# Performance work log

Measured on AMD Instinct MI355X. Metric: run time of the kernel, lower is better.

Reference implementation:

```python
import jax, jax.numpy as jnp
import numpy as np

B, S, D, H, DQ, DK = 2, 2048, 1024, 16, 64, 64


def setup_inputs() -> dict:
    key = jax.random.key(0)
    ks = jax.random.split(key, 11)
    s = 0.02
    return {
        "query": jax.random.normal(ks[0], (B, S, D), jnp.float32),
        "key": jax.random.normal(ks[1], (B, S, D), jnp.float32),
        "value": jax.random.normal(ks[2], (B, S, D), jnp.float32),
        "Wq": jax.random.normal(ks[3], (H, D, DQ), jnp.float32) * s,
        "bq": jax.random.normal(ks[4], (H, DQ), jnp.float32) * s,
        "Wk": jax.random.normal(ks[5], (H, D, DK), jnp.float32) * s,
        "bk": jax.random.normal(ks[6], (H, DK), jnp.float32) * s,
        "Wv": jax.random.normal(ks[7], (H, D, DK), jnp.float32) * s,
        "bv": jax.random.normal(ks[8], (H, DK), jnp.float32) * s,
        "Wo": jax.random.normal(ks[9], (H * DK, D), jnp.float32) * s,
        "bo": jax.random.normal(ks[10], (D,), jnp.float32) * s,
    }


def reference(query, key, value, Wq, bq, Wk, bk, Wv, bv, Wo, bo):
    # Per-head linear projections (batched over heads): [B,H,S,dq/dk]
    q = jnp.einsum('bsd,hde->bhse', query, Wq) + bq[None, :, None, :]
    k = jnp.einsum('bsd,hde->bhse', key, Wk) + bk[None, :, None, :]
    v = jnp.einsum('bsd,hde->bhse', value, Wv) + bv[None, :, None, :]
    # Scaled dot-product attention: softmax(QK^T / sqrt(dim_q)) V
    scale = 1.0 / jnp.sqrt(jnp.asarray(q.shape[-1], q.dtype))
    scores = jnp.einsum('bhse,bhte->bhst', q, k) * scale  # [B,H,S,S]
    attn = jax.nn.softmax(scores, axis=-1)
    out = jnp.einsum('bhst,bhte->bhse', attn, v)  # [B,H,S,dk]
    # Concat heads along feature dim, then output linear
    cat = out.transpose(0, 2, 1, 3).reshape(out.shape[0], out.shape[2], -1)  # [B,S,H*dk]
    return cat @ Wo + bo
```

## Files before the change

### kernel.cpp

```cpp
#include <hip/hip_runtime.h>
#include <hip/hip_bf16.h>
#include <math.h>

#define NB 2
#define NS 2048
#define ND 1024
#define NH 16
#define DH 64
#define MROWS (NB*NS)
#define NCOLS (NH*DH)

typedef __attribute__((ext_vector_type(8))) short bf16x8;
typedef __attribute__((ext_vector_type(4))) float f32x4;
typedef __attribute__((ext_vector_type(4))) unsigned short ushort4t;
typedef __attribute__((ext_vector_type(8))) unsigned short ushort8t;
typedef unsigned short ushort;

extern "C" __device__ float __ocml_native_exp2_f32(float);
#define EXP2F(x) __ocml_native_exp2_f32(x)
#define LOG2E 1.44269504088896f

static __device__ __forceinline__ ushort f2bf(float f) {
    union { __hip_bfloat16 b; ushort u; } cv;
    cv.b = __hip_bfloat16(f);
    return cv.u;
}

static __device__ __forceinline__ void gld_lds16(const void* g, void* l) {
    __builtin_amdgcn_global_load_lds(
        (const __attribute__((address_space(1))) void*)g,
        (__attribute__((address_space(3))) void*)l, 16, 0, 0);
}

__global__ __launch_bounds__(256) void convert_x(
    const float* __restrict__ q, const float* __restrict__ k,
    const float* __restrict__ v, ushort* __restrict__ X_bf)
{
    const size_t n1 = (size_t)MROWS * ND;
    const size_t off = ((size_t)blockIdx.x * 256 + threadIdx.x) * 8;
    const float* srcs[3] = {q, k, v};
    #pragma unroll
    for (int p = 0; p < 3; ++p) {
        float4 a = *(const float4*)(srcs[p] + off);
        float4 b = *(const float4*)(srcs[p] + off + 4);
        ushort8t w;
        w[0]=f2bf(a.x); w[1]=f2bf(a.y); w[2]=f2bf(a.z); w[3]=f2bf(a.w);
        w[4]=f2bf(b.x); w[5]=f2bf(b.y); w[6]=f2bf(b.z); w[7]=f2bf(b.w);
        *(ushort8t*)(X_bf + (size_t)p * n1 + off) = w;
    }
}

__global__ __launch_bounds__(256) void repack_w(
    const float* __restrict__ Wq, const float* __restrict__ Wk,
    const float* __restrict__ Wv, ushort* __restrict__ WT_bf)
{
    const int p = blockIdx.z;
    const float* W = (p == 0) ? Wq : (p == 1) ? Wk : Wv;
    const int h = blockIdx.y, d0 = blockIdx.x * 64;
    __shared__ float tile[64][65];
    const int t = threadIdx.x;
    {
        const int i = t >> 2, e0 = (t & 3) * 16;
        const float* src = W + ((size_t)h * ND + d0 + i) * DH + e0;
        #pragma unroll
        for (int u = 0; u < 4; ++u) {
            float4 v4 = ((const float4*)src)[u];
            tile[i][e0 + u*4 + 0] = v4.x; tile[i][e0 + u*4 + 1] = v4.y;
            tile[i][e0 + u*4 + 2] = v4.z; tile[i][e0 + u*4 + 3] = v4.w;
        }
    }
    __syncthreads();
    {
        const int e = t >> 2, dc = (t & 3) * 16;
        ushort* dst = WT_bf + ((size_t)p * NCOLS + h * 64 + e) * ND + d0 + dc;
        ushort8t w0, w1;
        #pragma unroll
        for (int u = 0; u < 8; ++u) { w0[u] = f2bf(tile[dc+u][e]); w1[u] = f2bf(tile[dc+8+u][e]); }
        *(ushort8t*)dst = w0;
        *(ushort8t*)(dst + 8) = w1;
    }
}

__global__ __launch_bounds__(256) void repack_wo(
    const float* __restrict__ Wo, ushort* __restrict__ WoT_bf)
{
    const int f0 = blockIdx.x * 64, c0 = blockIdx.y * 64;
    __shared__ float tile[64][65];
    const int t = threadIdx.x;
    {
        const int i = t >> 2, j0 = (t & 3) * 16;
        const float* src = Wo + (size_t)(f0 + i) * ND + c0 + j0;
        #pragma unroll
        for (int u = 0; u < 4; ++u) {
            float4 v4 = ((const float4*)src)[u];
            tile[i][j0 + u*4 + 0] = v4.x; tile[i][j0 + u*4 + 1] = v4.y;
            tile[i][j0 + u*4 + 2] = v4.z; tile[i][j0 + u*4 + 3] = v4.w;
        }
    }
    __syncthreads();
    {
        const int cl = t >> 2, fc = (t & 3) * 16;
        ushort* dst = WoT_bf + (size_t)(c0 + cl) * ND + f0 + fc;
        ushort8t w0, w1;
        #pragma unroll
        for (int u = 0; u < 8; ++u) { w0[u] = f2bf(tile[fc+u][cl]); w1[u] = f2bf(tile[fc+8+u][cl]); }
        *(ushort8t*)dst = w0;
        *(ushort8t*)(dst + 8) = w1;
    }
}

__global__ __launch_bounds__(256) void gemm_qkv(
    const ushort* __restrict__ X_bf, const ushort* __restrict__ WT_bf,
    const float* __restrict__ bq, const float* __restrict__ bk,
    const float* __restrict__ bv, ushort* __restrict__ qkv_bf)
{
    const int p = blockIdx.z;
    const float* bias = (p == 0) ? bq : (p == 1) ? bk : bv;
    const float scale = (p == 0) ? 0.125f * LOG2E : 1.0f;
    const int m0 = blockIdx.x * 128, n0 = blockIdx.y * 128;
    const int t = threadIdx.x, wid = t >> 6, lane = t & 63;
    const int wr = wid >> 1, wc = wid & 1;
    const int c = lane & 15, g = lane >> 4;

    __shared__ ushort ldsA[128 * 64];
    __shared__ ushort ldsB[128 * 64];

    const ushort* Ag = X_bf + (size_t)p * MROWS * ND + (size_t)m0 * ND;
    const ushort* Bg = WT_bf + (size_t)p * NCOLS * ND + (size_t)n0 * ND;

    f32x4 acc[4][4];
    #pragma unroll
    for (int m = 0; m < 4; ++m)
        #pragma unroll
        for (int n = 0; n < 4; ++n)
            acc[m][n] = (f32x4){0.f, 0.f, 0.f, 0.f};

    for (int k0 = 0; k0 < ND; k0 += 64) {
        __syncthreads();
        #pragma unroll
        for (int call = 0; call < 4; ++call) {
            const int chb = wid * 256 + call * 64;
            const int ch = chb + lane;
            const int row = ch >> 3, c16 = ch & 7;
            gld_lds16(Ag + (size_t)row * ND + k0 + c16 * 8, ldsA + (size_t)ch * 8);
            gld_lds16(Bg + (size_t)row * ND + k0 + c16 * 8, ldsB + (size_t)ch * 8);
        }
        __syncthreads();
        #pragma unroll
        for (int kc = 0; kc < 2; ++kc) {
            bf16x8 af[4], bfr[4];
            #pragma unroll
            for (int m = 0; m < 4; ++m)
                af[m] = *(const bf16x8*)(ldsA + (wr*64 + m*16 + c) * 64 + kc*32 + g*8);
            #pragma unroll
            for (int n = 0; n < 4; ++n)
                bfr[n] = *(const bf16x8*)(ldsB + (wc*64 + n*16 + c) * 64 + kc*32 + g*8);
            #pragma unroll
            for (int m = 0; m < 4; ++m)
                #pragma unroll
                for (int n = 0; n < 4; ++n)
                    acc[m][n] = __builtin_amdgcn_mfma_f32_16x16x32_bf16(af[m], bfr[n], acc[m][n], 0, 0, 0);
        }
    }

    ushort* dst = qkv_bf + (size_t)p * ((size_t)NB * NH * NS * DH);
    #pragma unroll
    for (int m = 0; m < 4; ++m) {
        const int gr0 = m0 + wr*64 + m*16 + g*4;
        #pragma unroll
        for (int n = 0; n < 4; ++n) {
            const int gc = n0 + wc*64 + n*16 + c;
            const int h = gc >> 6, e = gc & 63;
            const float bv_ = bias[gc];
            #pragma unroll
            for (int j = 0; j < 4; ++j) {
                const int r = gr0 + j;
                const int b = r >> 11, s = r & (NS - 1);
                dst[(((size_t)b * NH + h) * NS + s) * DH + e] = f2bf((acc[m][n][j] + bv_) * scale);
            }
        }
    }
}

__global__ __launch_bounds__(256) void v_transpose(
    const ushort* __restrict__ v_bf, ushort* __restrict__ vT_bf)
{
    const int bh = blockIdx.y, s0 = blockIdx.x * 256;
    __shared__ ushort tile[256][72];
    const int t = threadIdx.x;
    const ushort* src = v_bf + ((size_t)bh * NS + s0) * DH;
    #pragma unroll
    for (int u = 0; u < 8; ++u) {
        const int idx = u * 256 + t;
        const int row = idx >> 3, cc = (idx & 7) * 8;
        *(ushort8t*)&tile[row][cc] = *(const ushort8t*)(src + (size_t)row * DH + cc);
    }
    __syncthreads();
    const int e = t >> 2, sc = (t & 3) * 64;
    ushort* dst = vT_bf + ((size_t)bh * DH + e) * NS + s0 + sc;
    #pragma unroll
    for (int u = 0; u < 8; ++u) {
        ushort8t w;
        #pragma unroll
        for (int x = 0; x < 8; ++x) w[x] = tile[sc + u*8 + x][e];
        *(ushort8t*)(dst + u * 8) = w;
    }
}

__global__ __launch_bounds__(256) void attn_kernel(
    const ushort* __restrict__ q_bf, const ushort* __restrict__ k_bf,
    const ushort* __restrict__ vT_bf, ushort* __restrict__ cat_bf)
{
    __shared__ __attribute__((aligned(16))) char smem[40960];
    const int t = threadIdx.x;
    const int wid = t >> 6, lane = t & 63;
    const int g = lane >> 4, c = lane & 15;
    const int bh = blockIdx.y;
    const int qrow0 = blockIdx.x * 64 + wid * 16;

    bf16x8 qf[2];
    {
        const char* qp = (const char*)(q_bf + ((size_t)bh * NS + qrow0 + c) * DH);
        qf[0] = *(const bf16x8*)(qp + g * 16);
        qf[1] = *(const bf16x8*)(qp + 64 + g * 16);
    }

    f32x4 o_acc[4];
    const f32x4 zero = {0.f, 0.f, 0.f, 0.f};
    #pragma unroll
    for (int n = 0; n < 4; ++n) o_acc[n] = zero;
    float m[4], lsum[4];
    #pragma unroll
    for (int r = 0; r < 4; ++r) { m[r] = -INFINITY; lsum[r] = 0.f; }

    const char* kg = (const char*)(k_bf + (size_t)bh * NS * DH);
    const char* vg = (const char*)(vT_bf + (size_t)bh * DH * NS);

    const int ch0 = t * 2;
    const int row0 = ch0 >> 3, c16a = ch0 & 7;
    const int row1 = (ch0 + 1) >> 3, c16b = (ch0 + 1) & 7;
    const int swz0 = (c16a * 16) ^ ((row0 & 7) << 4);
    const int swz1 = (c16b * 16) ^ ((row1 & 7) << 4);

    ushort8t kr0, kr1, vr0, vr1;

    #define ATTN_LOAD(JT) do { \
        kr0 = *(const ushort8t*)(kg + (size_t)((JT) + row0) * 128 + c16a * 16); \
        kr1 = *(const ushort8t*)(kg + (size_t)((JT) + row1) * 128 + c16b * 16); \
        vr0 = *(const ushort8t*)(vg + (size_t)row0 * (NS*2) + (size_t)((JT) + c16a*8) * 2); \
        vr1 = *(const ushort8t*)(vg + (size_t)row1 * (NS*2) + (size_t)((JT) + c16b*8) * 2); \
    } while (0)

    #define ATTN_STORE(BUF) do { \
        char* Kd = smem + (BUF) * 8192; \
        char* Vd = smem + 16384 + (BUF) * 8192; \
        *(ushort8t*)(Kd + row0 * 128 + swz0) = kr0; \
        *(ushort8t*)(Kd + row1 * 128 + swz1) = kr1; \
        *(ushort8t*)(Vd + row0 * 128 + swz0) = vr0; \
        *(ushort8t*)(Vd + row1 * 128 + swz1) = vr1; \
    } while (0)

    ATTN_LOAD(0);
    ATTN_STORE(0);
    __syncthreads();
    int cur = 0;
    char* Ps = smem + 32768 + wid * 2048;

    for (int jt = 0; jt < NS; jt += 64) {
        ATTN_LOAD((jt + 64) & (NS - 1));

        const char* Ks  = smem + cur * 8192;
        const char* VTs = smem + 16384 + cur * 8192;

        f32x4 s_acc[4];
        #pragma unroll
        for (int n = 0; n < 4; ++n) s_acc[n] = zero;
        __builtin_amdgcn_s_setprio(1);
        #pragma unroll
        for (int n = 0; n < 4; ++n) {
            const int key = n * 16 + c;
            #pragma unroll
            for (int kc = 0; kc < 2; ++kc) {
                bf16x8 kf = *(const bf16x8*)(Ks + key * 128 + ((kc * 64 + g * 16) ^ ((key & 7) << 4)));
                s_acc[n] = __builtin_amdgcn_mfma_f32_16x16x32_bf16(qf[kc], kf, s_acc[n], 0, 0, 0);
            }
        }
        __builtin_amdgcn_s_setprio(0);

        float pv[4][4];
        #pragma unroll
        for (int r = 0; r < 4; ++r) {
            float tm = fmaxf(fmaxf(s_acc[0][r], s_acc[1][r]), fmaxf(s_acc[2][r], s_acc[3][r]));
            if (!__all(tm <= m[r] + 11.5f)) {
                tm = fmaxf(tm, __shfl_xor(tm, 1));
                tm = fmaxf(tm, __shfl_xor(tm, 2));
                tm = fmaxf(tm, __shfl_xor(tm, 4));
                tm = fmaxf(tm, __shfl_xor(tm, 8));
                const float mnew = fmaxf(m[r], tm);
                const float sc = EXP2F(m[r] - mnew);
                lsum[r] *= sc;
                o_acc[0][r] *= sc; o_acc[1][r] *= sc;
                o_acc[2][r] *= sc; o_acc[3][r] *= sc;
                m[r] = mnew;
            }
            float rs = 0.f;
            #pragma unroll
            for (int n = 0; n < 4; ++n) {
                float pj = EXP2F(s_acc[n][r] - m[r]);
                pv[n][r] = pj;
                rs += pj;
            }
            lsum[r] += rs;
        }

        #pragma unroll
        for (int n = 0; n < 4; ++n) {
            #pragma unroll
            for (int r = 0; r < 4; ++r) {
                const int q = g * 4 + r;
                *(ushort*)(Ps + q * 128 + ((n * 32 + c * 2) ^ ((q & 7) << 4))) = f2bf(pv[n][r]);
            }
        }

        __builtin_amdgcn_s_setprio(1);
        #pragma unroll
        for (int kc = 0; kc < 2; ++kc) {
            bf16x8 pa = *(const bf16x8*)(Ps + c * 128 + ((kc * 64 + g * 16) ^ ((c & 7) << 4)));
            #pragma unroll
            for (int n = 0; n < 4; ++n) {
                const int e = n * 16 + c;
                bf16x8 vf = *(const bf16x8*)(VTs + e * 128 + ((kc * 64 + g * 16) ^ ((e & 7) << 4)));
                o_acc[n] = __builtin_amdgcn_mfma_f32_16x16x32_bf16(pa, vf, o_acc[n], 0, 0, 0);
            }
        }
        __builtin_amdgcn_s_setprio(0);

        ATTN_STORE(cur ^ 1);
        __syncthreads();
        cur ^= 1;
    }

    #pragma unroll
    for (int r = 0; r < 4; ++r) {
        float rs = lsum[r];
        rs += __shfl_xor(rs, 1);
        rs += __shfl_xor(rs, 2);
        rs += __shfl_xor(rs, 4);
        rs += __shfl_xor(rs, 8);
        lsum[r] = rs;
    }

    const int b = bh >> 4, hh = bh & 15;
    ushort* op = cat_bf + (size_t)b * NS * NCOLS + hh * DH;
    #pragma unroll
    for (int r = 0; r < 4; ++r) {
        const float inv = 1.0f / lsum[r];
        const int srow = qrow0 + g * 4 + r;
        #pragma unroll
        for (int n = 0; n < 4; ++n)
            op[(size_t)srow * NCOLS + n * 16 + c] = f2bf(o_acc[n][r] * inv);
    }
    #undef ATTN_LOAD
    #undef ATTN_STORE
}

__global__ __launch_bounds__(256) void gemm_out(
    const ushort* __restrict__ cat_bf, const ushort* __restrict__ WoT_bf,
    const float* __restrict__ bo, float* __restrict__ out)
{
    const int m0 = blockIdx.x * 128, n0 = blockIdx.y * 128;
    const int t = threadIdx.x, wid = t >> 6, lane = t & 63;
    const int wr = wid >> 1, wc = wid & 1;
    const int c = lane & 15, g = lane >> 4;

    __shared__ ushort ldsA[128 * 64];
    __shared__ ushort ldsB[128 * 64];

    const ushort* Ag = cat_bf + (size_t)m0 * ND;
    const ushort* Bg = WoT_bf + (size_t)n0 * ND;

    f32x4 acc[4][4];
    #pragma unroll
    for (int m = 0; m < 4; ++m)
        #pragma unroll
        for (int n = 0; n < 4; ++n)
            acc[m][n] = (f32x4){0.f, 0.f, 0.f, 0.f};

    for (int k0 = 0; k0 < ND; k0 += 64) {
        __syncthreads();
        #pragma unroll
        for (int call = 0; call < 4; ++call) {
            const int chb = wid * 256 + call * 64;
            const int ch = chb + lane;
            const int row = ch >> 3, c16 = ch & 7;
            gld_lds16(Ag + (size_t)row * ND + k0 + c16 * 8, ldsA + (size_t)ch * 8);
            gld_lds16(Bg + (size_t)row * ND + k0 + c16 * 8, ldsB + (size_t)ch * 8);
        }
        __syncthreads();
        #pragma unroll
        for (int kc = 0; kc < 2; ++kc) {
            bf16x8 af[4], bfr[4];
            #pragma unroll
            for (int m = 0; m < 4; ++m)
                af[m] = *(const bf16x8*)(ldsA + (wr*64 + m*16 + c) * 64 + kc*32 + g*8);
            #pragma unroll
            for (int n = 0; n < 4; ++n)
                bfr[n] = *(const bf16x8*)(ldsB + (wc*64 + n*16 + c) * 64 + kc*32 + g*8);
            #pragma unroll
            for (int m = 0; m < 4; ++m)
                #pragma unroll
                for (int n = 0; n < 4; ++n)
                    acc[m][n] = __builtin_amdgcn_mfma_f32_16x16x32_bf16(af[m], bfr[n], acc[m][n], 0, 0, 0);
        }
    }

    #pragma unroll
    for (int m = 0; m < 4; ++m) {
        const int gr0 = m0 + wr*64 + m*16 + g*4;
        #pragma unroll
        for (int n = 0; n < 4; ++n) {
            const int gc = n0 + wc*64 + n*16 + c;
            const float bv_ = bo[gc];
            #pragma unroll
            for (int j = 0; j < 4; ++j)
                out[(size_t)(gr0 + j) * ND + gc] = acc[m][n][j] + bv_;
        }
    }
}

extern "C" void kernel_launch(void* const* d_in, const int* in_sizes, int n_in,
                              void* d_out, int out_size, void* d_ws, size_t ws_size,
                              hipStream_t stream) {
    const float* query = (const float*)d_in[0];
    const float* key_  = (const float*)d_in[1];
    const float* value = (const float*)d_in[2];
    const float* Wq = (const float*)d_in[3];
    const float* bq = (const float*)d_in[4];
    const float* Wk = (const float*)d_in[5];
    const float* bk = (const float*)d_in[6];
    const float* Wv = (const float*)d_in[7];
    const float* bv = (const float*)d_in[8];
    const float* Wo = (const float*)d_in[9];
    const float* bo = (const float*)d_in[10];
    float* out = (float*)d_out;

    const size_t per = (size_t)NB * NH * NS * DH;
    const size_t xsz = (size_t)MROWS * ND;

    ushort* X_bf   = (ushort*)d_ws;
    ushort* qkv_bf = X_bf + 3 * xsz;
    ushort* vT_bf  = qkv_bf + 3 * per;
    ushort* WT_bf  = vT_bf + per;
    ushort* WoT_bf = WT_bf + (size_t)3 * ND * NCOLS;
    ushort* cat_bf = X_bf;

    convert_x<<<2048, 256, 0, stream>>>(query, key_, value, X_bf);
    repack_w<<<dim3(16, 16, 3), 256, 0, stream>>>(Wq, Wk, Wv, WT_bf);
    repack_wo<<<dim3(16, 16), 256, 0, stream>>>(Wo, WoT_bf);

    gemm_qkv<<<dim3(32, 8, 3), 256, 0, stream>>>(X_bf, WT_bf, bq, bk, bv, qkv_bf);
    v_transpose<<<dim3(8, 32), 256, 0, stream>>>(qkv_bf + 2 * per, vT_bf);

    attn_kernel<<<dim3(32, 32), 256, 0, stream>>>(qkv_bf, qkv_bf + per, vT_bf, cat_bf);

    gemm_out<<<dim3(32, 8), 256, 0, stream>>>(cat_bf, WoT_bf, bo, out);
}
```

Measured before the change: 276.1 us.

## Use 512-thread attention blocks with 128 query rows and XCD-aware block mapping

The attention kernel now runs 8 waves per block covering 128 query rows, so each K/V tile staged in shared memory is reused by twice as many waves. Each thread now loads one K and one V chunk instead of two. A 1D grid is remapped so that consecutive blocks on the same XCD work on the same heads, aiming for better L2 locality of K/V. Shared memory grows to hold per-wave P buffers for 8 waves, which may reduce occupancy. The grid shrinks to 512 blocks, which may also leave some CUs underused.

Measured after the change: 274.8 us. About the same (-0.5%).

```diff
diff --git a/kernel.cpp b/kernel.cpp
--- a/kernel.cpp
+++ b/kernel.cpp
@@ -207,16 +207,21 @@
     }
 }
 
-__global__ __launch_bounds__(256) void attn_kernel(
+__global__ __launch_bounds__(512) void attn_kernel(
     const ushort* __restrict__ q_bf, const ushort* __restrict__ k_bf,
     const ushort* __restrict__ vT_bf, ushort* __restrict__ cat_bf)
 {
-    __shared__ __attribute__((aligned(16))) char smem[40960];
+    __shared__ __attribute__((aligned(16))) char smem[49152];
     const int t = threadIdx.x;
     const int wid = t >> 6, lane = t & 63;
     const int g = lane >> 4, c = lane & 15;
-    const int bh = blockIdx.y;
-    const int qrow0 = blockIdx.x * 64 + wid * 16;
+
+    const int linear = blockIdx.x;
+    const int xcd = linear & 7;
+    const int idx = linear >> 3;
+    const int bh = xcd * 4 + (idx >> 4);
+    const int qx = idx & 15;
+    const int qrow0 = qx * 128 + wid * 16;
 
     bf16x8 qf[2];
     {
@@ -236,28 +241,19 @@
     const char* kg = (const char*)(k_bf + (size_t)bh * NS * DH);
     const char* vg = (const char*)(vT_bf + (size_t)bh * DH * NS);
 
-    const int ch0 = t * 2;
-    const int row0 = ch0 >> 3, c16a = ch0 & 7;
-    const int row1 = (ch0 + 1) >> 3, c16b = (ch0 + 1) & 7;
-    const int swz0 = (c16a * 16) ^ ((row0 & 7) << 4);
-    const int swz1 = (c16b * 16) ^ ((row1 & 7) << 4);
-
-    ushort8t kr0, kr1, vr0, vr1;
+    const int row = t >> 3, c16 = t & 7;
+    const int swz = (c16 * 16) ^ ((row & 7) << 4);
+
+    ushort8t kr, vr;
 
     #define ATTN_LOAD(JT) do { \
-        kr0 = *(const ushort8t*)(kg + (size_t)((JT) + row0) * 128 + c16a * 16); \
-        kr1 = *(const ushort8t*)(kg + (size_t)((JT) + row1) * 128 + c16b * 16); \
-        vr0 = *(const ushort8t*)(vg + (size_t)row0 * (NS*2) + (size_t)((JT) + c16a*8) * 2); \
-        vr1 = *(const ushort8t*)(vg + (size_t)row1 * (NS*2) + (size_t)((JT) + c16b*8) * 2); \
+        kr = *(const ushort8t*)(kg + (size_t)((JT) + row) * 128 + c16 * 16); \
+        vr = *(const ushort8t*)(vg + (size_t)row * (NS*2) + (size_t)((JT) + c16*8) * 2); \
     } while (0)
 
     #define ATTN_STORE(BUF) do { \
-        char* Kd = smem + (BUF) * 8192; \
-        char* Vd = smem + 16384 + (BUF) * 8192; \
-        *(ushort8t*)(Kd + row0 * 128 + swz0) = kr0; \
-        *(ushort8t*)(Kd + row1 * 128 + swz1) = kr1; \
-        *(ushort8t*)(Vd + row0 * 128 + swz0) = vr0; \
-        *(ushort8t*)(Vd + row1 * 128 + swz1) = vr1; \
+        *(ushort8t*)(smem + (BUF) * 8192 + row * 128 + swz) = kr; \
+        *(ushort8t*)(smem + 16384 + (BUF) * 8192 + row * 128 + swz) = vr; \
     } while (0)
 
     ATTN_LOAD(0);
@@ -461,7 +457,7 @@
     gemm_qkv<<<dim3(32, 8, 3), 256, 0, stream>>>(X_bf, WT_bf, bq, bk, bv, qkv_bf);
     v_transpose<<<dim3(8, 32), 256, 0, stream>>>(qkv_bf + 2 * per, vT_bf);
 
-    attn_kernel<<<dim3(32, 32), 256, 0, stream>>>(qkv_bf, qkv_bf + per, vT_bf, cat_bf);
+    attn_kernel<<<512, 512, 0, stream>>>(qkv_bf, qkv_bf + per, vT_bf, cat_bf);
 
     gemm_out<<<dim3(32, 8), 256, 0, stream>>>(cat_bf, WoT_bf, bo, out);
 }
```

## Restructure attention to 32x32 MFMA with register-resident P and XCD-aware grid

Applied to the files above, without the earlier changes.

The attention kernel moves from 16x16x32 to 32x32x16 bf16 MFMA and computes S transposed (K as A operand), so each lane owns one query row. The softmax max/sum then needs only a cross-half shuffle. P is packed to bf16 in registers with v_cvt_pk and v_permlane32_swap rather than staged through LDS, which frees 8 KB of shared memory and removes the LDS write/read round trip. Each block now covers 128 query rows, and a 1D grid of 512 blocks is remapped so that blocks of the same head land on the same XCD for L2 reuse of K/V. The cost is more registers per thread (f32x16 accumulators) and half as many blocks, which lowers parallelism.

Result: faster. 249.3 us (-9.7%).

```diff
diff --git a/kernel.cpp b/kernel.cpp
--- a/kernel.cpp
+++ b/kernel.cpp
@@ -12,6 +12,7 @@
 
 typedef __attribute__((ext_vector_type(8))) short bf16x8;
 typedef __attribute__((ext_vector_type(4))) float f32x4;
+typedef __attribute__((ext_vector_type(16))) float f32x16;
 typedef __attribute__((ext_vector_type(4))) unsigned short ushort4t;
 typedef __attribute__((ext_vector_type(8))) unsigned short ushort8t;
 typedef unsigned short ushort;
@@ -24,6 +25,12 @@
     union { __hip_bfloat16 b; ushort u; } cv;
     cv.b = __hip_bfloat16(f);
     return cv.u;
+}
+
+static __device__ __forceinline__ unsigned cvtpk(float a, float b) {
+    unsigned r;
+    asm("v_cvt_pk_bf16_f32 %0, %1, %2" : "=v"(r) : "v"(a), "v"(b));
+    return r;
 }
 
 static __device__ __forceinline__ void gld_lds16(const void* g, void* l) {
@@ -211,60 +218,66 @@
     const ushort* __restrict__ q_bf, const ushort* __restrict__ k_bf,
     const ushort* __restrict__ vT_bf, ushort* __restrict__ cat_bf)
 {
-    __shared__ __attribute__((aligned(16))) char smem[40960];
+    __shared__ __attribute__((aligned(16))) char smem[32768];
     const int t = threadIdx.x;
     const int wid = t >> 6, lane = t & 63;
-    const int g = lane >> 4, c = lane & 15;
-    const int bh = blockIdx.y;
-    const int qrow0 = blockIdx.x * 64 + wid * 16;
-
-    bf16x8 qf[2];
+    const int ql = lane & 31;
+    const int hi = lane >> 5;
+
+    const int linear = blockIdx.x;
+    const int xcd = linear & 7;
+    const int idx = linear >> 3;
+    const int bh = xcd * 4 + (idx >> 4);
+    const int qx = idx & 15;
+    const int qrow0 = qx * 128 + wid * 32;
+
+    bf16x8 qf[4];
     {
-        const char* qp = (const char*)(q_bf + ((size_t)bh * NS + qrow0 + c) * DH);
-        qf[0] = *(const bf16x8*)(qp + g * 16);
-        qf[1] = *(const bf16x8*)(qp + 64 + g * 16);
-    }
-
-    f32x4 o_acc[4];
-    const f32x4 zero = {0.f, 0.f, 0.f, 0.f};
-    #pragma unroll
-    for (int n = 0; n < 4; ++n) o_acc[n] = zero;
-    float m[4], lsum[4];
-    #pragma unroll
-    for (int r = 0; r < 4; ++r) { m[r] = -INFINITY; lsum[r] = 0.f; }
+        const char* qp = (const char*)(q_bf + ((size_t)bh * NS + qrow0 + ql) * DH);
+        #pragma unroll
+        for (int ds = 0; ds < 4; ++ds)
+            qf[ds] = *(const bf16x8*)(qp + ds * 32 + hi * 16);
+    }
+
+    f32x16 o_acc[2];
+    #pragma unroll
+    for (int et = 0; et < 2; ++et)
+        #pragma unroll
+        for (int i = 0; i < 16; ++i)
+            o_acc[et][i] = 0.f;
+    float m = -INFINITY, lsum = 0.f;
 
     const char* kg = (const char*)(k_bf + (size_t)bh * NS * DH);
     const char* vg = (const char*)(vT_bf + (size_t)bh * DH * NS);
 
     const int ch0 = t * 2;
     const int row0 = ch0 >> 3, c16a = ch0 & 7;
-    const int row1 = (ch0 + 1) >> 3, c16b = (ch0 + 1) & 7;
+    const int c16b = c16a + 1;
     const int swz0 = (c16a * 16) ^ ((row0 & 7) << 4);
-    const int swz1 = (c16b * 16) ^ ((row1 & 7) << 4);
+    const int swz1 = (c16b * 16) ^ ((row0 & 7) << 4);
 
     ushort8t kr0, kr1, vr0, vr1;
 
     #define ATTN_LOAD(JT) do { \
         kr0 = *(const ushort8t*)(kg + (size_t)((JT) + row0) * 128 + c16a * 16); \
-        kr1 = *(const ushort8t*)(kg + (size_t)((JT) + row1) * 128 + c16b * 16); \
+        kr1 = *(const ushort8t*)(kg + (size_t)((JT) + row0) * 128 + c16b * 16); \
         vr0 = *(const ushort8t*)(vg + (size_t)row0 * (NS*2) + (size_t)((JT) + c16a*8) * 2); \
-        vr1 = *(const ushort8t*)(vg + (size_t)row1 * (NS*2) + (size_t)((JT) + c16b*8) * 2); \
+        vr1 = *(const ushort8t*)(vg + (size_t)row0 * (NS*2) + (size_t)((JT) + c16b*8) * 2); \
     } while (0)
 
     #define ATTN_STORE(BUF) do { \
         char* Kd = smem + (BUF) * 8192; \
         char* Vd = smem + 16384 + (BUF) * 8192; \
         *(ushort8t*)(Kd + row0 * 128 + swz0) = kr0; \
-        *(ushort8t*)(Kd + row1 * 128 + swz1) = kr1; \
+        *(ushort8t*)(Kd + row0 * 128 + swz1) = kr1; \
         *(ushort8t*)(Vd + row0 * 128 + swz0) = vr0; \
-        *(ushort8t*)(Vd + row1 * 128 + swz1) = vr1; \
+        *(ushort8t*)(Vd + row0 * 128 + swz1) = vr1; \
     } while (0)
 
     ATTN_LOAD(0);
     ATTN_STORE(0);
     __syncthreads();
     int cur = 0;
-    char* Ps = smem + 32768 + wid * 2048;
 
     for (int jt = 0; jt < NS; jt += 64) {
         ATTN_LOAD((jt + 64) & (NS - 1));
@@ -272,93 +285,101 @@
         const char* Ks  = smem + cur * 8192;
         const char* VTs = smem + 16384 + cur * 8192;
 
-        f32x4 s_acc[4];
-        #pragma unroll
-        for (int n = 0; n < 4; ++n) s_acc[n] = zero;
+        f32x16 s_acc[2];
+        #pragma unroll
+        for (int kt = 0; kt < 2; ++kt)
+            #pragma unroll
+            for (int i = 0; i < 16; ++i)
+                s_acc[kt][i] = 0.f;
         __builtin_amdgcn_s_setprio(1);
         #pragma unroll
-        for (int n = 0; n < 4; ++n) {
-            const int key = n * 16 + c;
-            #pragma unroll
-            for (int kc = 0; kc < 2; ++kc) {
-                bf16x8 kf = *(const bf16x8*)(Ks + key * 128 + ((kc * 64 + g * 16) ^ ((key & 7) << 4)));
-                s_acc[n] = __builtin_amdgcn_mfma_f32_16x16x32_bf16(qf[kc], kf, s_acc[n], 0, 0, 0);
+        for (int ds = 0; ds < 4; ++ds) {
+            #pragma unroll
+            for (int kt = 0; kt < 2; ++kt) {
+                const int key = kt * 32 + ql;
+                bf16x8 kf = *(const bf16x8*)(Ks + key * 128 + ((ds*32 + hi*16) ^ ((key & 7) << 4)));
+                s_acc[kt] = __builtin_amdgcn_mfma_f32_32x32x16_bf16(kf, qf[ds], s_acc[kt], 0, 0, 0);
             }
         }
         __builtin_amdgcn_s_setprio(0);
 
-        float pv[4][4];
-        #pragma unroll
-        for (int r = 0; r < 4; ++r) {
-            float tm = fmaxf(fmaxf(s_acc[0][r], s_acc[1][r]), fmaxf(s_acc[2][r], s_acc[3][r]));
-            if (!__all(tm <= m[r] + 11.5f)) {
-                tm = fmaxf(tm, __shfl_xor(tm, 1));
-                tm = fmaxf(tm, __shfl_xor(tm, 2));
-                tm = fmaxf(tm, __shfl_xor(tm, 4));
-                tm = fmaxf(tm, __shfl_xor(tm, 8));
-                const float mnew = fmaxf(m[r], tm);
-                const float sc = EXP2F(m[r] - mnew);
-                lsum[r] *= sc;
-                o_acc[0][r] *= sc; o_acc[1][r] *= sc;
-                o_acc[2][r] *= sc; o_acc[3][r] *= sc;
-                m[r] = mnew;
+        float tm = -INFINITY;
+        #pragma unroll
+        for (int kt = 0; kt < 2; ++kt)
+            #pragma unroll
+            for (int i = 0; i < 16; ++i)
+                tm = fmaxf(tm, s_acc[kt][i]);
+        if (!__all(tm <= m + 11.5f)) {
+            const float tm2 = fmaxf(tm, __shfl_xor(tm, 32));
+            const float mnew = fmaxf(m, tm2);
+            const float sc = EXP2F(m - mnew);
+            lsum *= sc;
+            #pragma unroll
+            for (int et = 0; et < 2; ++et)
+                #pragma unroll
+                for (int i = 0; i < 16; ++i)
+                    o_acc[et][i] *= sc;
+            m = mnew;
+        }
+
+        float rs = 0.f;
+        #pragma unroll
+        for (int kt = 0; kt < 2; ++kt) {
+            float pe[16];
+            #pragma unroll
+            for (int i = 0; i < 16; ++i) {
+                pe[i] = EXP2F(s_acc[kt][i] - m);
+                rs += pe[i];
             }
-            float rs = 0.f;
-            #pragma unroll
-            for (int n = 0; n < 4; ++n) {
-                float pj = EXP2F(s_acc[n][r] - m[r]);
-                pv[n][r] = pj;
-                rs += pj;
+            unsigned a0 = cvtpk(pe[0],  pe[1]);
+            unsigned a1 = cvtpk(pe[2],  pe[3]);
+            unsigned b0 = cvtpk(pe[4],  pe[5]);
+            unsigned b1 = cvtpk(pe[6],  pe[7]);
+            asm volatile("v_permlane32_swap_b32 %0, %1" : "+v"(a0), "+v"(b0));
+            asm volatile("v_permlane32_swap_b32 %0, %1" : "+v"(a1), "+v"(b1));
+            unsigned c0 = cvtpk(pe[8],  pe[9]);
+            unsigned c1 = cvtpk(pe[10], pe[11]);
+            unsigned d0 = cvtpk(pe[12], pe[13]);
+            unsigned d1 = cvtpk(pe[14], pe[15]);
+            asm volatile("v_permlane32_swap_b32 %0, %1" : "+v"(c0), "+v"(d0));
+            asm volatile("v_permlane32_swap_b32 %0, %1" : "+v"(c1), "+v"(d1));
+            union { bf16x8 v; unsigned u[4]; } B0, B1;
+            B0.u[0] = a0; B0.u[1] = a1; B0.u[2] = b0; B0.u[3] = b1;
+            B1.u[0] = c0; B1.u[1] = c1; B1.u[2] = d0; B1.u[3] = d1;
+
+            __builtin_amdgcn_s_setprio(1);
+            #pragma unroll
+            for (int et = 0; et < 2; ++et) {
+                const int e = et * 32 + ql;
+                bf16x8 vf0 = *(const bf16x8*)(VTs + e * 128 + (((2*kt)   * 32 + hi*16) ^ ((e & 7) << 4)));
+                o_acc[et] = __builtin_amdgcn_mfma_f32_32x32x16_bf16(vf0, B0.v, o_acc[et], 0, 0, 0);
+                bf16x8 vf1 = *(const bf16x8*)(VTs + e * 128 + (((2*kt+1) * 32 + hi*16) ^ ((e & 7) << 4)));
+                o_acc[et] = __builtin_amdgcn_mfma_f32_32x32x16_bf16(vf1, B1.v, o_acc[et], 0, 0, 0);
             }
-            lsum[r] += rs;
-        }
-
-        #pragma unroll
-        for (int n = 0; n < 4; ++n) {
-            #pragma unroll
-            for (int r = 0; r < 4; ++r) {
-                const int q = g * 4 + r;
-                *(ushort*)(Ps + q * 128 + ((n * 32 + c * 2) ^ ((q & 7) << 4))) = f2bf(pv[n][r]);
-            }
-        }
-
-        __builtin_amdgcn_s_setprio(1);
-        #pragma unroll
-        for (int kc = 0; kc < 2; ++kc) {
-            bf16x8 pa = *(const bf16x8*)(Ps + c * 128 + ((kc * 64 + g * 16) ^ ((c & 7) << 4)));
-            #pragma unroll
-            for (int n = 0; n < 4; ++n) {
-                const int e = n * 16 + c;
-                bf16x8 vf = *(const bf16x8*)(VTs + e * 128 + ((kc * 64 + g * 16) ^ ((e & 7) << 4)));
-                o_acc[n] = __builtin_amdgcn_mfma_f32_16x16x32_bf16(pa, vf, o_acc[n], 0, 0, 0);
-            }
-        }
-        __builtin_amdgcn_s_setprio(0);
+            __builtin_amdgcn_s_setprio(0);
+        }
+        lsum += rs;
 
         ATTN_STORE(cur ^ 1);
         __syncthreads();
         cur ^= 1;
     }
 
-    #pragma unroll
-    for (int r = 0; r < 4; ++r) {
-        float rs = lsum[r];
-        rs += __shfl_xor(rs, 1);
-        rs += __shfl_xor(rs, 2);
-        rs += __shfl_xor(rs, 4);
-        rs += __shfl_xor(rs, 8);
-        lsum[r] = rs;
-    }
+    lsum += __shfl_xor(lsum, 32);
+    const float inv = 1.0f / lsum;
 
     const int b = bh >> 4, hh = bh & 15;
-    ushort* op = cat_bf + (size_t)b * NS * NCOLS + hh * DH;
-    #pragma unroll
-    for (int r = 0; r < 4; ++r) {
-        const float inv = 1.0f / lsum[r];
-        const int srow = qrow0 + g * 4 + r;
-        #pragma unroll
-        for (int n = 0; n < 4; ++n)
-            op[(size_t)srow * NCOLS + n * 16 + c] = f2bf(o_acc[n][r] * inv);
+    const int s = qrow0 + ql;
+    ushort* op = cat_bf + ((size_t)b * NS + s) * NCOLS + hh * DH;
+    #pragma unroll
+    for (int et = 0; et < 2; ++et) {
+        #pragma unroll
+        for (int rgrp = 0; rgrp < 4; ++rgrp) {
+            uint2 wv;
+            wv.x = cvtpk(o_acc[et][rgrp*4+0] * inv, o_acc[et][rgrp*4+1] * inv);
+            wv.y = cvtpk(o_acc[et][rgrp*4+2] * inv, o_acc[et][rgrp*4+3] * inv);
+            *(uint2*)(op + et*32 + rgrp*8 + hi*4) = wv;
+        }
     }
     #undef ATTN_LOAD
     #undef ATTN_STORE
@@ -461,7 +482,7 @@
     gemm_qkv<<<dim3(32, 8, 3), 256, 0, stream>>>(X_bf, WT_bf, bq, bk, bv, qkv_bf);
     v_transpose<<<dim3(8, 32), 256, 0, stream>>>(qkv_bf + 2 * per, vT_bf);
 
-    attn_kernel<<<dim3(32, 32), 256, 0, stream>>>(qkv_bf, qkv_bf + per, vT_bf, cat_bf);
+    attn_kernel<<<512, 256, 0, stream>>>(qkv_bf, qkv_bf + per, vT_bf, cat_bf);
 
     gemm_out<<<dim3(32, 8), 256, 0, stream>>>(cat_bf, WoT_bf, bo, out);
 }
```
